# Optimization experiments

Hardware: AMD Instinct MI355X
Metric: run time of the kernel (lower is better)

The kernel has to match this reference:

```python
import jax, jax.numpy as jnp
import numpy as np

NUM_GROUPS = 32
EPS = 1e-6


def setup_inputs() -> dict:
    key = jax.random.key(0)
    ks = jax.random.split(key, 6)
    n, t, c, h, w = 2, 5, 64, 128, 128
    K = 512  # codebook size
    return {
        "x": jax.random.normal(ks[0], (n, t, c, h, w), dtype=jnp.float32),
        "mb": jax.random.normal(ks[1], (c, K), dtype=jnp.float32),
        "phi_w": jax.random.normal(ks[2], (c, c), dtype=jnp.float32) * (1.0 / np.sqrt(c)),
        "phi_b": jax.random.normal(ks[3], (c,), dtype=jnp.float32) * 0.01,
        "gn_w": jnp.ones((c,), dtype=jnp.float32),
        "gn_b": jnp.zeros((c,), dtype=jnp.float32),
        "wz_w": jax.random.normal(ks[4], (c, c), dtype=jnp.float32) * (1.0 / np.sqrt(c)),
        "wz_b": jax.random.normal(ks[5], (c,), dtype=jnp.float32) * 0.01,
    }


def reference(x, mb, phi_w, phi_b, gn_w, gn_b, wz_w, wz_b):
    n, t, c, h, w = x.shape
    B = n * t
    xf = x.reshape(B, c, h, w)

    # GroupNorm(32 groups, eps=1e-6, affine)
    xg = xf.reshape(B, NUM_GROUPS, c // NUM_GROUPS, h, w)
    mu = jnp.mean(xg, axis=(2, 3, 4), keepdims=True)
    var = jnp.var(xg, axis=(2, 3, 4), keepdims=True)
    xn = ((xg - mu) * jax.lax.rsqrt(var + EPS)).reshape(B, c, h, w)
    xn = xn * gn_w[:, None, None] + gn_b[:, None, None]

    # 1x1 conv phi, flatten spatial -> tokens (B, HW, C)
    phi = jnp.einsum('oc,bchw->bohw', phi_w, xn) + phi_b[:, None, None]
    p = phi.reshape(B, c, h * w).transpose(0, 2, 1)

    # soft-VQ attention against codebook mb (C, K)
    scores = jnp.einsum('bnc,ck->bnk', p, mb) * (c ** -0.5)
    attn = jax.nn.softmax(scores, axis=-1)
    y = jnp.einsum('bnk,ck->bnc', attn, mb)  # (B, HW, C)

    y = y.transpose(0, 2, 1).reshape(B, c, h, w)
    out = jnp.einsum('oc,bchw->bohw', wz_w, y) + wz_b[:, None, None] + xf
    return out.reshape(n, t, c, h, w)
```

## Files before the change

kernel.cpp:

```cpp
#include <hip/hip_runtime.h>


#define HWN 16384
#define CCH 64

using short8 = __attribute__((ext_vector_type(8))) short;
using f32x4  = __attribute__((ext_vector_type(4))) float;

__device__ __forceinline__ ushort f2bf(float f) {
    union { float f; unsigned int i; } v; v.f = f;
    return (ushort)((v.i + 0x8000u) >> 16);
}
__device__ __forceinline__ unsigned int pk2(float a, float b) {
    return (unsigned int)f2bf(a) | ((unsigned int)f2bf(b) << 16);
}

__global__ void prep_kernel(const float* __restrict__ mb,
                            const float* __restrict__ phiw,
                            const float* __restrict__ wzw,
                            ushort* __restrict__ ws) {
    int i = blockIdx.x * 256 + threadIdx.x;
    int j = i & 7, lane = (i >> 3) & 63, m = lane & 15, q = lane >> 4;
    if (i < 32768) {
        int t = i >> 9;
        int tile = t >> 1, s = t & 1;
        ws[i] = f2bf(mb[(s * 32 + q * 8 + j) * 512 + tile * 16 + m]);
    } else if (i < 65536) {
        int t = (i - 32768) >> 9;
        int mt = t & 3, u2 = t >> 2, s2 = u2 & 1, cc = u2 >> 1;
        ws[i] = f2bf(mb[(mt * 16 + m) * 512 + cc * 64 + s2 * 32 + q * 8 + j]);
    } else if (i < 69632) {
        int t = (i - 65536) >> 9;
        int mt = t >> 1, s = t & 1;
        ws[i] = f2bf(phiw[(mt * 16 + m) * 64 + s * 32 + q * 8 + j]);
    } else {
        int t = (i - 69632) >> 9;
        int mt = t >> 1, s = t & 1;
        ws[i] = f2bf(wzw[(mt * 16 + m) * 64 + s * 32 + q * 8 + j]);
    }
}

__global__ __launch_bounds__(256) void stats_kernel(const float* __restrict__ x,
                                                    float* __restrict__ wsf) {
    int b = blockIdx.x >> 5;
    int g = blockIdx.x & 31;
    const float4* b4 = (const float4*)(x + (size_t)b * CCH * HWN + (size_t)(g * 2) * HWN);
    float s = 0.f, s2 = 0.f;
    for (int i = threadIdx.x; i < 8192; i += 256) {
        float4 u = b4[i];
        s  += (u.x + u.y) + (u.z + u.w);
        s2 += (u.x*u.x + u.y*u.y) + (u.z*u.z + u.w*u.w);
    }
    for (int off = 32; off > 0; off >>= 1) {
        s  += __shfl_down(s, off);
        s2 += __shfl_down(s2, off);
    }
    __shared__ float rs[4], rs2[4];
    int wave = threadIdx.x >> 6, lane = threadIdx.x & 63;
    if (lane == 0) { rs[wave] = s; rs2[wave] = s2; }
    __syncthreads();
    if (threadIdx.x == 0) {
        float ts  = rs[0] + rs[1] + rs[2] + rs[3];
        float ts2 = rs2[0] + rs2[1] + rs2[2] + rs2[3];
        float mu  = ts * (1.f / 32768.f);
        float var = ts2 * (1.f / 32768.f) - mu * mu;
        wsf[36864 + b * 32 + g] = mu;
        wsf[37184 + b * 32 + g] = rsqrtf(var + 1e-6f);
    }
}

__global__ __launch_bounds__(256, 4) void main_mfma(
    const float* __restrict__ x, const ushort* __restrict__ ws,
    const float* __restrict__ phib, const float* __restrict__ gnw,
    const float* __restrict__ gnb, const float* __restrict__ wzb,
    float* __restrict__ out)
{
    const int lane = threadIdx.x & 63, wv = threadIdx.x >> 6;
    const int m = lane & 15, q = lane >> 4;
    const int blk = blockIdx.x;
    const int b   = blk >> 7;
    const int hw0 = ((blk & 127) << 7) + (wv << 5);

    const ushort* mbA  = ws;
    const ushort* mbY  = ws + 32768;
    const ushort* phiA = ws + 65536;
    const ushort* wzA  = ws + 69632;
    const float*  statf = (const float*)(ws + 73728);

    __shared__ ushort Sl[4][32 * 72];
    ushort* Sw = &Sl[wv][0];

    const float* xb = x + (size_t)b * CCH * HWN;

    short8 bx[2][2];
#pragma unroll
    for (int s = 0; s < 2; ++s) {
        const int cbase = s * 32 + q * 8;
        f32x4 mu4 = *(const f32x4*)(statf + b * 32 + (cbase >> 1));
        f32x4 rs4 = *(const f32x4*)(statf + 320 + b * 32 + (cbase >> 1));
        f32x4 gwv0 = *(const f32x4*)(gnw + cbase), gwv1 = *(const f32x4*)(gnw + cbase + 4);
        f32x4 gbv0 = *(const f32x4*)(gnb + cbase), gbv1 = *(const f32x4*)(gnb + cbase + 4);
#pragma unroll
        for (int n = 0; n < 2; ++n)
#pragma unroll
        for (int j = 0; j < 8; ++j) {
            float v  = xb[(size_t)(cbase + j) * HWN + hw0 + n * 16 + m];
            float gw = (j < 4) ? gwv0[j & 3] : gwv1[j & 3];
            float gb = (j < 4) ? gbv0[j & 3] : gbv1[j & 3];
            float xn = (v - mu4[j >> 1]) * rs4[j >> 1] * gw + gb;
            bx[n][s][j] = (short)f2bf(xn);
        }
    }

#pragma unroll
    for (int mt = 0; mt < 4; ++mt) {
        f32x4 a0 = {0.f,0.f,0.f,0.f}, a1 = {0.f,0.f,0.f,0.f};
#pragma unroll
        for (int s = 0; s < 2; ++s) {
            short8 ap = *(const short8*)(phiA + (((mt * 2 + s) * 64 + lane) << 3));
            a0 = __builtin_amdgcn_mfma_f32_16x16x32_bf16(ap, bx[0][s], a0, 0, 0, 0);
            a1 = __builtin_amdgcn_mfma_f32_16x16x32_bf16(ap, bx[1][s], a1, 0, 0, 0);
        }
        f32x4 pb = *(const f32x4*)(phib + mt * 16 + q * 4);
        uint2 w0 = make_uint2(pk2(a0[0]+pb[0], a0[1]+pb[1]), pk2(a0[2]+pb[2], a0[3]+pb[3]));
        uint2 w1 = make_uint2(pk2(a1[0]+pb[0], a1[1]+pb[1]), pk2(a1[2]+pb[2], a1[3]+pb[3]));
        *(uint2*)(Sw + m * 72 + mt * 16 + q * 4)        = w0;
        *(uint2*)(Sw + (16 + m) * 72 + mt * 16 + q * 4) = w1;
    }

    short8 bp[2][2];
#pragma unroll
    for (int n = 0; n < 2; ++n)
#pragma unroll
    for (int s = 0; s < 2; ++s)
        bp[n][s] = *(const short8*)(Sw + (n * 16 + m) * 72 + s * 32 + q * 8);

    f32x4 accY[2][4];
#pragma unroll
    for (int n = 0; n < 2; ++n)
#pragma unroll
    for (int mt = 0; mt < 4; ++mt) accY[n][mt] = (f32x4){0.f,0.f,0.f,0.f};
    float l0 = 0.f, l1 = 0.f;

    for (int cc = 0; cc < 8; ++cc) {
#pragma unroll
        for (int u = 0; u < 4; ++u) {
            f32x4 s0 = {0.f,0.f,0.f,0.f}, s1 = {0.f,0.f,0.f,0.f};
#pragma unroll
            for (int s = 0; s < 2; ++s) {
                short8 am = *(const short8*)(mbA + ((((cc * 4 + u) * 2 + s) * 64 + lane) << 3));
                s0 = __builtin_amdgcn_mfma_f32_16x16x32_bf16(am, bp[0][s], s0, 0, 0, 0);
                s1 = __builtin_amdgcn_mfma_f32_16x16x32_bf16(am, bp[1][s], s1, 0, 0, 0);
            }
            float e00 = __expf(s0[0]*0.125f), e01 = __expf(s0[1]*0.125f);
            float e02 = __expf(s0[2]*0.125f), e03 = __expf(s0[3]*0.125f);
            float e10 = __expf(s1[0]*0.125f), e11 = __expf(s1[1]*0.125f);
            float e12 = __expf(s1[2]*0.125f), e13 = __expf(s1[3]*0.125f);
            l0 += (e00 + e01) + (e02 + e03);
            l1 += (e10 + e11) + (e12 + e13);
            *(uint2*)(Sw + m * 72 + u * 16 + q * 4)        = make_uint2(pk2(e00,e01), pk2(e02,e03));
            *(uint2*)(Sw + (16 + m) * 72 + u * 16 + q * 4) = make_uint2(pk2(e10,e11), pk2(e12,e13));
        }
#pragma unroll
        for (int s2 = 0; s2 < 2; ++s2) {
            short8 be0 = *(const short8*)(Sw + m * 72 + s2 * 32 + q * 8);
            short8 be1 = *(const short8*)(Sw + (16 + m) * 72 + s2 * 32 + q * 8);
#pragma unroll
            for (int mt = 0; mt < 4; ++mt) {
                short8 ay = *(const short8*)(mbY + ((((cc * 2 + s2) * 4 + mt) * 64 + lane) << 3));
                accY[0][mt] = __builtin_amdgcn_mfma_f32_16x16x32_bf16(ay, be0, accY[0][mt], 0, 0, 0);
                accY[1][mt] = __builtin_amdgcn_mfma_f32_16x16x32_bf16(ay, be1, accY[1][mt], 0, 0, 0);
            }
        }
    }

    l0 += __shfl_xor(l0, 16); l0 += __shfl_xor(l0, 32);
    l1 += __shfl_xor(l1, 16); l1 += __shfl_xor(l1, 32);
    const float li0 = 1.f / l0, li1 = 1.f / l1;

#pragma unroll
    for (int mt = 0; mt < 4; ++mt) {
        *(uint2*)(Sw + m * 72 + mt * 16 + q * 4) =
            make_uint2(pk2(accY[0][mt][0], accY[0][mt][1]), pk2(accY[0][mt][2], accY[0][mt][3]));
        *(uint2*)(Sw + (16 + m) * 72 + mt * 16 + q * 4) =
            make_uint2(pk2(accY[1][mt][0], accY[1][mt][1]), pk2(accY[1][mt][2], accY[1][mt][3]));
    }
    short8 by[2][2];
#pragma unroll
    for (int n = 0; n < 2; ++n)
#pragma unroll
    for (int s = 0; s < 2; ++s)
        by[n][s] = *(const short8*)(Sw + (n * 16 + m) * 72 + s * 32 + q * 8);

    float* ob = out + (size_t)b * CCH * HWN;
#pragma unroll
    for (int mt = 0; mt < 4; ++mt) {
        f32x4 c0 = {0.f,0.f,0.f,0.f}, c1 = {0.f,0.f,0.f,0.f};
#pragma unroll
        for (int s = 0; s < 2; ++s) {
            short8 aw = *(const short8*)(wzA + (((mt * 2 + s) * 64 + lane) << 3));
            c0 = __builtin_amdgcn_mfma_f32_16x16x32_bf16(aw, by[0][s], c0, 0, 0, 0);
            c1 = __builtin_amdgcn_mfma_f32_16x16x32_bf16(aw, by[1][s], c1, 0, 0, 0);
        }
        f32x4 wb = *(const f32x4*)(wzb + mt * 16 + q * 4);
#pragma unroll
        for (int r = 0; r < 4; ++r) {
            int o = mt * 16 + q * 4 + r;
            size_t base = (size_t)o * HWN + hw0 + m;
            ob[base]      = c0[r] * li0 + wb[r] + xb[base];
            ob[base + 16] = c1[r] * li1 + wb[r] + xb[base + 16];
        }
    }
}

extern "C" void kernel_launch(void* const* d_in, const int* in_sizes, int n_in,
                              void* d_out, int out_size, void* d_ws, size_t ws_size,
                              hipStream_t stream) {
    const float* x    = (const float*)d_in[0];
    const float* mb   = (const float*)d_in[1];
    const float* phiw = (const float*)d_in[2];
    const float* phib = (const float*)d_in[3];
    const float* gnw  = (const float*)d_in[4];
    const float* gnb  = (const float*)d_in[5];
    const float* wzw  = (const float*)d_in[6];
    const float* wzb  = (const float*)d_in[7];

    const int B = in_sizes[0] / (CCH * HWN);

    prep_kernel<<<288, 256, 0, stream>>>(mb, phiw, wzw, (ushort*)d_ws);
    stats_kernel<<<B * 32, 256, 0, stream>>>(x, (float*)d_ws);
    main_mfma<<<B * 128, 256, 0, stream>>>(x, (const ushort*)d_ws,
                                           phib, gnw, gnb, wzb, (float*)d_out);
}
```

Before: 184.8 us.

## Widen per-wave token tile to 64, double-buffer LDS, merge prep and stats kernels

```diff
diff --git a/kernel.cpp b/kernel.cpp
--- a/kernel.cpp
+++ b/kernel.cpp
@@ -15,33 +15,31 @@
     return (unsigned int)f2bf(a) | ((unsigned int)f2bf(b) << 16);
 }
 
-__global__ void prep_kernel(const float* __restrict__ mb,
-                            const float* __restrict__ phiw,
-                            const float* __restrict__ wzw,
-                            ushort* __restrict__ ws) {
-    int i = blockIdx.x * 256 + threadIdx.x;
-    int j = i & 7, lane = (i >> 3) & 63, m = lane & 15, q = lane >> 4;
-    if (i < 32768) {
-        int t = i >> 9;
-        int tile = t >> 1, s = t & 1;
-        ws[i] = f2bf(mb[(s * 32 + q * 8 + j) * 512 + tile * 16 + m]);
-    } else if (i < 65536) {
-        int t = (i - 32768) >> 9;
-        int mt = t & 3, u2 = t >> 2, s2 = u2 & 1, cc = u2 >> 1;
-        ws[i] = f2bf(mb[(mt * 16 + m) * 512 + cc * 64 + s2 * 32 + q * 8 + j]);
-    } else if (i < 69632) {
-        int t = (i - 65536) >> 9;
-        int mt = t >> 1, s = t & 1;
-        ws[i] = f2bf(phiw[(mt * 16 + m) * 64 + s * 32 + q * 8 + j]);
-    } else {
-        int t = (i - 69632) >> 9;
-        int mt = t >> 1, s = t & 1;
-        ws[i] = f2bf(wzw[(mt * 16 + m) * 64 + s * 32 + q * 8 + j]);
-    }
-}
-
-__global__ __launch_bounds__(256) void stats_kernel(const float* __restrict__ x,
-                                                    float* __restrict__ wsf) {
+__global__ __launch_bounds__(256) void prep_stats_kernel(
+    const float* __restrict__ x, const float* __restrict__ mb,
+    const float* __restrict__ phiw, const float* __restrict__ wzw,
+    ushort* __restrict__ ws, int nstat)
+{
+    if (blockIdx.x >= nstat) {
+        int i = (blockIdx.x - nstat) * 256 + threadIdx.x;
+        int j = i & 7, lane = (i >> 3) & 63, m = lane & 15, q = lane >> 4;
+        if (i < 32768) {
+            int t = i >> 9, tile = t >> 1, s = t & 1;
+            ws[i] = f2bf(mb[(s * 32 + q * 8 + j) * 512 + tile * 16 + m]);
+        } else if (i < 65536) {
+            int t = (i - 32768) >> 9;
+            int mt = t & 3, u2 = t >> 2, s2 = u2 & 1, cc = u2 >> 1;
+            ws[i] = f2bf(mb[(mt * 16 + m) * 512 + cc * 64 + s2 * 32 + q * 8 + j]);
+        } else if (i < 69632) {
+            int t = (i - 65536) >> 9, mt = t >> 1, s = t & 1;
+            ws[i] = f2bf(phiw[(mt * 16 + m) * 64 + s * 32 + q * 8 + j]);
+        } else {
+            int t = (i - 69632) >> 9, mt = t >> 1, s = t & 1;
+            ws[i] = f2bf(wzw[(mt * 16 + m) * 64 + s * 32 + q * 8 + j]);
+        }
+        return;
+    }
+    float* wsf = (float*)ws;
     int b = blockIdx.x >> 5;
     int g = blockIdx.x & 31;
     const float4* b4 = (const float4*)(x + (size_t)b * CCH * HWN + (size_t)(g * 2) * HWN);
@@ -69,7 +67,7 @@
     }
 }
 
-__global__ __launch_bounds__(256, 4) void main_mfma(
+__global__ __launch_bounds__(128, 2) void main_mfma(
     const float* __restrict__ x, const ushort* __restrict__ ws,
     const float* __restrict__ phib, const float* __restrict__ gnw,
     const float* __restrict__ gnb, const float* __restrict__ wzb,
@@ -79,7 +77,7 @@
     const int m = lane & 15, q = lane >> 4;
     const int blk = blockIdx.x;
     const int b   = blk >> 7;
-    const int hw0 = ((blk & 127) << 7) + (wv << 5);
+    const int hw0 = ((blk & 127) << 7) + (wv << 6);
 
     const ushort* mbA  = ws;
     const ushort* mbY  = ws + 32768;
@@ -87,12 +85,13 @@
     const ushort* wzA  = ws + 69632;
     const float*  statf = (const float*)(ws + 73728);
 
-    __shared__ ushort Sl[4][32 * 72];
-    ushort* Sw = &Sl[wv][0];
+    __shared__ ushort Sl[2][2][64 * 72];
+    ushort* E0 = &Sl[wv][0][0];
+    ushort* E1 = &Sl[wv][1][0];
 
     const float* xb = x + (size_t)b * CCH * HWN;
 
-    short8 bx[2][2];
+    short8 bx[4][2];
 #pragma unroll
     for (int s = 0; s < 2; ++s) {
         const int cbase = s * 32 + q * 8;
@@ -101,7 +100,7 @@
         f32x4 gwv0 = *(const f32x4*)(gnw + cbase), gwv1 = *(const f32x4*)(gnw + cbase + 4);
         f32x4 gbv0 = *(const f32x4*)(gnb + cbase), gbv1 = *(const f32x4*)(gnb + cbase + 4);
 #pragma unroll
-        for (int n = 0; n < 2; ++n)
+        for (int n = 0; n < 4; ++n)
 #pragma unroll
         for (int j = 0; j < 8; ++j) {
             float v  = xb[(size_t)(cbase + j) * HWN + hw0 + n * 16 + m];
@@ -114,101 +113,119 @@
 
 #pragma unroll
     for (int mt = 0; mt < 4; ++mt) {
-        f32x4 a0 = {0.f,0.f,0.f,0.f}, a1 = {0.f,0.f,0.f,0.f};
+        f32x4 a[4];
+#pragma unroll
+        for (int n = 0; n < 4; ++n) a[n] = (f32x4){0.f,0.f,0.f,0.f};
 #pragma unroll
         for (int s = 0; s < 2; ++s) {
             short8 ap = *(const short8*)(phiA + (((mt * 2 + s) * 64 + lane) << 3));
-            a0 = __builtin_amdgcn_mfma_f32_16x16x32_bf16(ap, bx[0][s], a0, 0, 0, 0);
-            a1 = __builtin_amdgcn_mfma_f32_16x16x32_bf16(ap, bx[1][s], a1, 0, 0, 0);
+#pragma unroll
+            for (int n = 0; n < 4; ++n)
+                a[n] = __builtin_amdgcn_mfma_f32_16x16x32_bf16(ap, bx[n][s], a[n], 0, 0, 0);
         }
         f32x4 pb = *(const f32x4*)(phib + mt * 16 + q * 4);
-        uint2 w0 = make_uint2(pk2(a0[0]+pb[0], a0[1]+pb[1]), pk2(a0[2]+pb[2], a0[3]+pb[3]));
-        uint2 w1 = make_uint2(pk2(a1[0]+pb[0], a1[1]+pb[1]), pk2(a1[2]+pb[2], a1[3]+pb[3]));
-        *(uint2*)(Sw + m * 72 + mt * 16 + q * 4)        = w0;
-        *(uint2*)(Sw + (16 + m) * 72 + mt * 16 + q * 4) = w1;
-    }
-
-    short8 bp[2][2];
-#pragma unroll
-    for (int n = 0; n < 2; ++n)
+#pragma unroll
+        for (int n = 0; n < 4; ++n)
+            *(uint2*)(E0 + (n * 16 + m) * 72 + mt * 16 + q * 4) =
+                make_uint2(pk2(a[n][0]+pb[0], a[n][1]+pb[1]), pk2(a[n][2]+pb[2], a[n][3]+pb[3]));
+    }
+
+    short8 bp[4][2];
+#pragma unroll
+    for (int n = 0; n < 4; ++n)
 #pragma unroll
     for (int s = 0; s < 2; ++s)
-        bp[n][s] = *(const short8*)(Sw + (n * 16 + m) * 72 + s * 32 + q * 8);
-
-    f32x4 accY[2][4];
-#pragma unroll
-    for (int n = 0; n < 2; ++n)
+        bp[n][s] = *(const short8*)(E0 + (n * 16 + m) * 72 + s * 32 + q * 8);
+
+    f32x4 accY[4][4];
+#pragma unroll
+    for (int n = 0; n < 4; ++n)
 #pragma unroll
     for (int mt = 0; mt < 4; ++mt) accY[n][mt] = (f32x4){0.f,0.f,0.f,0.f};
-    float l0 = 0.f, l1 = 0.f;
-
-    for (int cc = 0; cc < 8; ++cc) {
+    float lsum[4] = {0.f, 0.f, 0.f, 0.f};
+
+    auto chunk = [&](int cc, ushort* Eb) {
 #pragma unroll
         for (int u = 0; u < 4; ++u) {
-            f32x4 s0 = {0.f,0.f,0.f,0.f}, s1 = {0.f,0.f,0.f,0.f};
-#pragma unroll
-            for (int s = 0; s < 2; ++s) {
-                short8 am = *(const short8*)(mbA + ((((cc * 4 + u) * 2 + s) * 64 + lane) << 3));
-                s0 = __builtin_amdgcn_mfma_f32_16x16x32_bf16(am, bp[0][s], s0, 0, 0, 0);
-                s1 = __builtin_amdgcn_mfma_f32_16x16x32_bf16(am, bp[1][s], s1, 0, 0, 0);
+            short8 am0 = *(const short8*)(mbA + ((((cc * 4 + u) * 2 + 0) * 64 + lane) << 3));
+            short8 am1 = *(const short8*)(mbA + ((((cc * 4 + u) * 2 + 1) * 64 + lane) << 3));
+#pragma unroll
+            for (int n = 0; n < 4; ++n) {
+                f32x4 sa = {0.f,0.f,0.f,0.f};
+                sa = __builtin_amdgcn_mfma_f32_16x16x32_bf16(am0, bp[n][0], sa, 0, 0, 0);
+                sa = __builtin_amdgcn_mfma_f32_16x16x32_bf16(am1, bp[n][1], sa, 0, 0, 0);
+                float e0 = __expf(sa[0] * 0.125f), e1 = __expf(sa[1] * 0.125f);
+                float e2 = __expf(sa[2] * 0.125f), e3 = __expf(sa[3] * 0.125f);
+                lsum[n] += (e0 + e1) + (e2 + e3);
+                *(uint2*)(Eb + (n * 16 + m) * 72 + u * 16 + q * 4) =
+                    make_uint2(pk2(e0, e1), pk2(e2, e3));
             }
-            float e00 = __expf(s0[0]*0.125f), e01 = __expf(s0[1]*0.125f);
-            float e02 = __expf(s0[2]*0.125f), e03 = __expf(s0[3]*0.125f);
-            float e10 = __expf(s1[0]*0.125f), e11 = __expf(s1[1]*0.125f);
-            float e12 = __expf(s1[2]*0.125f), e13 = __expf(s1[3]*0.125f);
-            l0 += (e00 + e01) + (e02 + e03);
-            l1 += (e10 + e11) + (e12 + e13);
-            *(uint2*)(Sw + m * 72 + u * 16 + q * 4)        = make_uint2(pk2(e00,e01), pk2(e02,e03));
-            *(uint2*)(Sw + (16 + m) * 72 + u * 16 + q * 4) = make_uint2(pk2(e10,e11), pk2(e12,e13));
         }
 #pragma unroll
         for (int s2 = 0; s2 < 2; ++s2) {
-            short8 be0 = *(const short8*)(Sw + m * 72 + s2 * 32 + q * 8);
-            short8 be1 = *(const short8*)(Sw + (16 + m) * 72 + s2 * 32 + q * 8);
+            short8 be[4];
+#pragma unroll
+            for (int n = 0; n < 4; ++n)
+                be[n] = *(const short8*)(Eb + (n * 16 + m) * 72 + s2 * 32 + q * 8);
 #pragma unroll
             for (int mt = 0; mt < 4; ++mt) {
                 short8 ay = *(const short8*)(mbY + ((((cc * 2 + s2) * 4 + mt) * 64 + lane) << 3));
-                accY[0][mt] = __builtin_amdgcn_mfma_f32_16x16x32_bf16(ay, be0, accY[0][mt], 0, 0, 0);
-                accY[1][mt] = __builtin_amdgcn_mfma_f32_16x16x32_bf16(ay, be1, accY[1][mt], 0, 0, 0);
+#pragma unroll
+                for (int n = 0; n < 4; ++n)
+                    accY[n][mt] = __builtin_amdgcn_mfma_f32_16x16x32_bf16(ay, be[n], accY[n][mt], 0, 0, 0);
             }
         }
-    }
-
-    l0 += __shfl_xor(l0, 16); l0 += __shfl_xor(l0, 32);
-    l1 += __shfl_xor(l1, 16); l1 += __shfl_xor(l1, 32);
-    const float li0 = 1.f / l0, li1 = 1.f / l1;
-
+    };
+
+    for (int ccp = 0; ccp < 4; ++ccp) {
+        chunk(2 * ccp,     E0);
+        chunk(2 * ccp + 1, E1);
+    }
+
+    float linv[4];
+#pragma unroll
+    for (int n = 0; n < 4; ++n) {
+        float l = lsum[n];
+        l += __shfl_xor(l, 16);
+        l += __shfl_xor(l, 32);
+        linv[n] = 1.f / l;
+    }
+
+#pragma unroll
+    for (int mt = 0; mt < 4; ++mt)
+#pragma unroll
+    for (int n = 0; n < 4; ++n)
+        *(uint2*)(E0 + (n * 16 + m) * 72 + mt * 16 + q * 4) =
+            make_uint2(pk2(accY[n][mt][0], accY[n][mt][1]), pk2(accY[n][mt][2], accY[n][mt][3]));
+
+    short8 by[4][2];
+#pragma unroll
+    for (int n = 0; n < 4; ++n)
+#pragma unroll
+    for (int s = 0; s < 2; ++s)
+        by[n][s] = *(const short8*)(E0 + (n * 16 + m) * 72 + s * 32 + q * 8);
+
+    float* ob = out + (size_t)b * CCH * HWN;
 #pragma unroll
     for (int mt = 0; mt < 4; ++mt) {
-        *(uint2*)(Sw + m * 72 + mt * 16 + q * 4) =
-            make_uint2(pk2(accY[0][mt][0], accY[0][mt][1]), pk2(accY[0][mt][2], accY[0][mt][3]));
-        *(uint2*)(Sw + (16 + m) * 72 + mt * 16 + q * 4) =
-            make_uint2(pk2(accY[1][mt][0], accY[1][mt][1]), pk2(accY[1][mt][2], accY[1][mt][3]));
-    }
-    short8 by[2][2];
-#pragma unroll
-    for (int n = 0; n < 2; ++n)
-#pragma unroll
-    for (int s = 0; s < 2; ++s)
-        by[n][s] = *(const short8*)(Sw + (n * 16 + m) * 72 + s * 32 + q * 8);
-
-    float* ob = out + (size_t)b * CCH * HWN;
-#pragma unroll
-    for (int mt = 0; mt < 4; ++mt) {
-        f32x4 c0 = {0.f,0.f,0.f,0.f}, c1 = {0.f,0.f,0.f,0.f};
+        f32x4 c[4];
+#pragma unroll
+        for (int n = 0; n < 4; ++n) c[n] = (f32x4){0.f,0.f,0.f,0.f};
 #pragma unroll
         for (int s = 0; s < 2; ++s) {
             short8 aw = *(const short8*)(wzA + (((mt * 2 + s) * 64 + lane) << 3));
-            c0 = __builtin_amdgcn_mfma_f32_16x16x32_bf16(aw, by[0][s], c0, 0, 0, 0);
-            c1 = __builtin_amdgcn_mfma_f32_16x16x32_bf16(aw, by[1][s], c1, 0, 0, 0);
+#pragma unroll
+            for (int n = 0; n < 4; ++n)
+                c[n] = __builtin_amdgcn_mfma_f32_16x16x32_bf16(aw, by[n][s], c[n], 0, 0, 0);
         }
         f32x4 wb = *(const f32x4*)(wzb + mt * 16 + q * 4);
 #pragma unroll
         for (int r = 0; r < 4; ++r) {
             int o = mt * 16 + q * 4 + r;
             size_t base = (size_t)o * HWN + hw0 + m;
-            ob[base]      = c0[r] * li0 + wb[r] + xb[base];
-            ob[base + 16] = c1[r] * li1 + wb[r] + xb[base + 16];
+#pragma unroll
+            for (int n = 0; n < 4; ++n)
+                ob[base + n * 16] = c[n][r] * linv[n] + wb[r] + xb[base + n * 16];
         }
     }
 }
@@ -227,8 +244,8 @@
 
     const int B = in_sizes[0] / (CCH * HWN);
 
-    prep_kernel<<<288, 256, 0, stream>>>(mb, phiw, wzw, (ushort*)d_ws);
-    stats_kernel<<<B * 32, 256, 0, stream>>>(x, (float*)d_ws);
-    main_mfma<<<B * 128, 256, 0, stream>>>(x, (const ushort*)d_ws,
+    prep_stats_kernel<<<B * 32 + 288, 256, 0, stream>>>(x, mb, phiw, wzw,
+                                                        (ushort*)d_ws, B * 32);
+    main_mfma<<<B * 128, 128, 0, stream>>>(x, (const ushort*)d_ws,
                                            phib, gnw, gnb, wzb, (float*)d_out);
 }
```

After: 190.5 us. 1.03x slower.
